# Kernel optimization log

Measured on AMD Instinct MI355X. Metric: run time of the kernel, lower is better.

## Reference

```python
import jax, jax.numpy as jnp
from jax import lax
import numpy as np

LRELU_SLOPE = 0.01  # PyTorch LeakyReLU default
BETA = 0.25


def lrelu(x):
    return jnp.where(x >= 0, x, LRELU_SLOPE * x)


def conv2d(x, w, b, stride, pad):
    # x: [B,C,H,W], w: [Cout,Cin,k,k] (torch OIHW)
    y = lax.conv_general_dilated(x, w, (stride, stride), ((pad, pad), (pad, pad)),
                                 dimension_numbers=('NCHW', 'OIHW', 'NCHW'))
    return y + b[None, :, None, None]


def conv_transpose2d(x, w, b, stride, out_pad):
    # w: torch ConvTranspose2d weight [Cin,Cout,k,k]; implement as dilated conv
    # with spatially flipped kernel. out = (i-1)*stride + k + out_pad.
    wf = jnp.flip(w, (2, 3)).transpose(1, 0, 2, 3)  # -> [Cout,Cin,k,k]
    k = w.shape[2]
    pad = ((k - 1, k - 1 + out_pad), (k - 1, k - 1 + out_pad))
    y = lax.conv_general_dilated(x, wf, (1, 1), pad, lhs_dilation=(stride, stride),
                                 dimension_numbers=('NCHW', 'OIHW', 'NCHW'))
    return y + b[None, :, None, None]


def setup_inputs() -> dict:
    key = jax.random.key(0)
    ks = jax.random.split(key, 16)
    s = 0.05
    inp = {
        'x':   jax.random.normal(ks[0], (64, 1, 256, 256), jnp.float32),
        'ew1': jax.random.normal(ks[1], (8, 1, 4, 4), jnp.float32) * s,
        'eb1': jnp.zeros((8,), jnp.float32),
        'ew2': jax.random.normal(ks[2], (16, 8, 4, 4), jnp.float32) * s,
        'eb2': jnp.zeros((16,), jnp.float32),
        'ew3': jax.random.normal(ks[3], (32, 16, 4, 4), jnp.float32) * s,
        'eb3': jnp.zeros((32,), jnp.float32),
        'ew4': jax.random.normal(ks[4], (32, 32, 3, 3), jnp.float32) * s,
        'eb4': jnp.zeros((32,), jnp.float32),
        'ew5': jax.random.normal(ks[5], (64, 32, 1, 1), jnp.float32) * s,
        'eb5': jnp.zeros((64,), jnp.float32),
        'dw1': jax.random.normal(ks[6], (32, 64, 3, 3), jnp.float32) * s,
        'db1': jnp.zeros((32,), jnp.float32),
        'dw2': jax.random.normal(ks[7], (32, 16, 4, 4), jnp.float32) * s,
        'db2': jnp.zeros((16,), jnp.float32),
        'dw3': jax.random.normal(ks[8], (16, 8, 4, 4), jnp.float32) * s,
        'db3': jnp.zeros((8,), jnp.float32),
        'dw4': jax.random.normal(ks[9], (8, 1, 4, 4), jnp.float32) * s,
        'db4': jnp.zeros((1,), jnp.float32),
        # nn.init.uniform_(-1/K, 1/K) with K=512
        'codebook': jax.random.uniform(ks[10], (512, 64), jnp.float32,
                                       minval=-1.0 / 512, maxval=1.0 / 512),
    }
    return inp


def vqvae_forward(x, ew1, eb1, ew2, eb2, ew3, eb3, ew4, eb4, ew5, eb5,
                  dw1, db1, dw2, db2, dw3, db3, dw4, db4, codebook):
    # ---- encoder ----
    h = lrelu(conv2d(x, ew1, eb1, 2, 0))   # [B,8,127,127]
    h = lrelu(conv2d(h, ew2, eb2, 2, 0))   # [B,16,62,62]
    h = lrelu(conv2d(h, ew3, eb3, 2, 0))   # [B,32,30,30]
    h = lrelu(conv2d(h, ew4, eb4, 1, 1))   # [B,32,30,30]
    h = lrelu(conv2d(h, ew5, eb5, 1, 0))   # [B,64,30,30]
    # ---- vector quantizer ----
    lat = h.transpose(0, 2, 3, 1)                      # [B,h,w,D]
    D = lat.shape[-1]
    flat = lat.reshape(-1, D)                          # [N,D]
    # squared euclidean distances via expansion (same argmin as torch.norm)
    d2 = (jnp.sum(flat * flat, axis=1, keepdims=True)
          - 2.0 * flat @ codebook.T
          + jnp.sum(codebook * codebook, axis=1))      # [N,K]
    idx = jnp.argmin(d2, axis=1)                       # [N]
    q = codebook[idx].reshape(lat.shape)               # [B,h,w,D]
    commitment = jnp.mean((lax.stop_gradient(q) - lat) ** 2)
    embedding = jnp.mean((q - lax.stop_gradient(lat)) ** 2)
    vq_loss = commitment * BETA + embedding
    q_st = lat + lax.stop_gradient(q - lat)            # straight-through
    z = q_st.transpose(0, 3, 1, 2)                     # [B,D,h,w]
    # ---- decoder ----
    h = lrelu(conv2d(z, dw1, db1, 1, 1))               # [B,32,30,30]
    h = lrelu(conv_transpose2d(h, dw2, db2, 2, 1))     # [B,16,63,63]
    h = lrelu(conv_transpose2d(h, dw3, db3, 2, 1))     # [B,8,131,131]
    recons = jnp.tanh(conv_transpose2d(h, dw4, db4, 2, 0))  # [B,1,264,264]
    return recons, vq_loss


def reference(x, ew1, eb1, ew2, eb2, ew3, eb3, ew4, eb4, ew5, eb5,
              dw1, db1, dw2, db2, dw3, db3, dw4, db4, codebook):
    return vqvae_forward(x, ew1, eb1, ew2, eb2, ew3, eb3, ew4, eb4, ew5, eb5,
                         dw1, db1, dw2, db2, dw3, db3, dw4, db4, codebook)
```

## Files before the change

### kernel.cpp

```cpp
#include <hip/hip_runtime.h>
#include <hip/hip_bf16.h>
#include <math.h>

#define LRELU 0.01f

template<int NW>
__device__ __forceinline__ void ldw(const float* p, float* w) {
    if constexpr (NW % 4 == 0) {
#pragma unroll
        for (int u = 0; u < NW / 4; u++) {
            float4 v = *(const float4*)(p + 4 * u);
            w[4*u] = v.x; w[4*u+1] = v.y; w[4*u+2] = v.z; w[4*u+3] = v.w;
        }
    } else {
#pragma unroll
        for (int c = 0; c < NW; c++) w[c] = p[c];
    }
}

__device__ __forceinline__ void wfwd(const float* s, float* d, int CIN, int COUT,
                                     int KK, int i) {
    int co = i / (CIN * KK); int r = i - co * CIN * KK;
    int ci = r / KK; int t = r - ci * KK;
    d[(ci * KK + t) * COUT + co] = s[i];
}
__device__ __forceinline__ void wtr(const float* s, float* d, int CIN, int COUT,
                                    int KK, int i) {
    int ci = i / (COUT * KK); int r = i - ci * COUT * KK;
    int co = r / KK; int t = r - co * KK;
    d[(t * CIN + ci) * COUT + co] = s[i];
}
__global__ __launch_bounds__(256)
void prep_k(const float* e1, const float* e2, const float* e3, const float* e4,
            const float* e5, const float* d1, const float* d2, const float* d3,
            const float* d4, float* w, const float* cbp, float* hcbn,
            unsigned long long* keys, float* loss, int* idxm, int N) {
    int i = blockIdx.x * 256 + threadIdx.x;
    if      (i < 128)   wfwd(e1, w + 0,     1,  8, 16, i);
    else if (i < 2176)  wfwd(e2, w + 128,   8, 16, 16, i - 128);
    else if (i < 10368) wfwd(e3, w + 2176, 16, 32, 16, i - 2176);
    else if (i < 19584) wfwd(e4, w + 10368, 32, 32, 9, i - 10368);
    else if (i < 21632) wfwd(e5, w + 19584, 32, 64, 1, i - 19584);
    else if (i < 40064) wfwd(d1, w + 21632, 64, 32, 9, i - 21632);
    else if (i < 48256) wtr (d2, w + 40064, 32, 16, 16, i - 40064);
    else if (i < 50304) wtr (d3, w + 48256, 16,  8, 16, i - 48256);
    else if (i < 50432) wtr (d4, w + 50304,  8,  1, 16, i - 50304);
    else if (i < 50944) {
        int k = i - 50432;
        const float* c = cbp + k * 64;
        float s = 0.f;
#pragma unroll
        for (int d = 0; d < 64; d++) s = fmaf(c[d], c[d], s);
        hcbn[k] = 0.5f * s;
    } else if (i < 50944 + N) {
        keys[i - 50944] = 0xFFFFFFFFFFFFFFFFull;
    } else if (i == 50944 + N) {
        loss[0] = 0.f;
    } else if (i < 50945 + N + 64 * 124) {
        int j = i - (50945 + N);
        int b2 = j / 124, s = j - b2 * 124;
        int r, c;
        if (s < 32)      { r = 0;  c = s; }
        else if (s < 64) { r = 31; c = s - 32; }
        else { int u = s - 64; r = 1 + (u >> 1); c = (u & 1) * 31; }
        idxm[b2 * 1024 + r * 32 + c] = 512;
    }
}

__global__ __launch_bounds__(256)
void ubuild_k(const float* __restrict__ w, const float* __restrict__ cb,
              float* __restrict__ U) {
    int g = blockIdx.x * 256 + threadIdx.x;
    if (g >= 513 * 288) return;
    if (g >= 512 * 288) { U[g] = 0.f; return; }
    int k = g / 288, rem = g - k * 288;
    const float* cr = cb + k * 64;
    float s = 0.f;
#pragma unroll 4
    for (int ci = 0; ci < 64; ci++)
        s = fmaf(w[ci * 288 + rem], cr[ci], s);
    U[g] = s;
}

template<int CIN, int COUT, int CO_BLK, int HIN, int ISTR, int HOUT, int WOUT,
         int OPLANE, int OSTR, int OPAD, int CB, int RB, int ZCONV, int ZF_CH>
__global__ __launch_bounds__(256)
void convs2_k(const float* __restrict__ in, const float* __restrict__ wt,
              const float* __restrict__ bias, float* __restrict__ out) {
    const int b = blockIdx.x, cog = blockIdx.y, tid = threadIdx.x;
    if (ZF_CH > 0 && (int)blockIdx.z >= ZCONV) {
        if (cog != 0) return;
        int i = ((int)blockIdx.z - ZCONV) * 256 + tid;
        if (i >= ZF_CH * 124) return;
        int ch = i / 124, s = i - ch * 124;
        int r, c;
        if (s < 32)      { r = 0;  c = s; }
        else if (s < 64) { r = 31; c = s - 32; }
        else { int u = s - 64; r = 1 + (u >> 1); c = (u & 1) * 31; }
        out[(size_t)(b * ZF_CH + ch) * 1024 + r * 32 + c] = 0.f;
        return;
    }
    __shared__ __align__(16) float lw[CIN * 16 * CO_BLK];
    for (int i = tid; i < CIN * 16 * CO_BLK; i += 256) {
        int row = i / CO_BLK, c = i - row * CO_BLK;
        lw[i] = wt[row * COUT + cog * CO_BLK + c];
    }
    __syncthreads();

    const int tz = blockIdx.z;
    const int cbi = tz / RB, rb = tz - cbi * RB;
    const int tx = tid & 15, ty = tid >> 4;
    const int ow0 = (cbi * 16 + tx) * 2;
    const int oh  = rb * 16 + ty;
    if (oh >= HOUT || ow0 >= WOUT) return;
    const bool p1v = (ow0 + 1) < WOUT;

    float acc[CO_BLK][2];
#pragma unroll
    for (int c = 0; c < CO_BLK; c++) {
        float bv = bias[cog * CO_BLK + c];
        acc[c][0] = bv; acc[c][1] = bv;
    }
    const float* inb = in + ((size_t)(b * CIN) * HIN + oh * 2) * ISTR + ow0 * 2;
#pragma unroll 2
    for (int ci = 0; ci < CIN; ci++) {
        const float* r = inb + (size_t)ci * HIN * ISTR;
        float4 a4[4]; float2 b2[4];
#pragma unroll
        for (int kh = 0; kh < 4; kh++) {
            a4[kh] = *(const float4*)(r + kh * ISTR);
            b2[kh] = p1v ? *(const float2*)(r + kh * ISTR + 4) : make_float2(0.f, 0.f);
        }
        const float* wr = lw + ci * 16 * CO_BLK;
#pragma unroll
        for (int kh = 0; kh < 4; kh++) {
            float x0[4] = {a4[kh].x, a4[kh].y, a4[kh].z, a4[kh].w};
            float x1[4] = {a4[kh].z, a4[kh].w, b2[kh].x, b2[kh].y};
#pragma unroll
            for (int kw = 0; kw < 4; kw++) {
                float wv[CO_BLK];
                ldw<CO_BLK>(wr + (kh * 4 + kw) * CO_BLK, wv);
#pragma unroll
                for (int c = 0; c < CO_BLK; c++) {
                    acc[c][0] = fmaf(x0[kw], wv[c], acc[c][0]);
                    acc[c][1] = fmaf(x1[kw], wv[c], acc[c][1]);
                }
            }
        }
    }
    float* ob = out + (size_t)(b * COUT + cog * CO_BLK) * OPLANE
                    + (oh + OPAD) * OSTR + ow0 + OPAD;
#pragma unroll
    for (int c = 0; c < CO_BLK; c++) {
        float v0 = acc[c][0]; v0 = (v0 >= 0.f) ? v0 : LRELU * v0;
        ob[(size_t)c * OPLANE] = v0;
        if (p1v) {
            float v1 = acc[c][1]; v1 = (v1 >= 0.f) ? v1 : LRELU * v1;
            ob[(size_t)c * OPLANE + 1] = v1;
        }
    }
}

template<int CIN, int COUT, int CO_BLK, int OPLANE, int OSTR, int OPADH, int OPADV,
         bool ZSIDE>
__global__ __launch_bounds__(256)
void conv3_k(const float* __restrict__ in, const float* __restrict__ wt,
             const float* __restrict__ bias, float* __restrict__ out) {
    const int b = blockIdx.x, cog = blockIdx.y, tid = threadIdx.x;
    __shared__ __align__(16) float lw[CIN * 9 * CO_BLK];
    for (int i = tid; i < CIN * 9 * CO_BLK; i += 256) {
        int row = i / CO_BLK, c = i - row * CO_BLK;
        lw[i] = wt[row * COUT + cog * CO_BLK + c];
    }
    __syncthreads();

    const int rb = blockIdx.z;
    const int tx = tid & 15, ty = tid >> 4;
    const int r = rb * 16 + ty;
    if (r >= 30) return;
    const int ow0 = tx * 2;
    if (tx == 15) {
        if (ZSIDE) {
#pragma unroll
            for (int c = 0; c < CO_BLK; c++) {
                float* base = out + (size_t)(b * COUT + cog * CO_BLK + c) * OPLANE
                                  + (r + OPADV) * OSTR;
                base[0] = 0.f; base[31] = 0.f; base[32] = 0.f;
            }
        }
        return;
    }
    float acc[CO_BLK][2];
#pragma unroll
    for (int c = 0; c < CO_BLK; c++) {
        float bv = bias[cog * CO_BLK + c];
        acc[c][0] = bv; acc[c][1] = bv;
    }
    const float* inb = in + ((size_t)(b * CIN) * 32 + r) * 32 + ow0;
#pragma unroll 2
    for (int ci = 0; ci < CIN; ci++) {
        const float* rr = inb + (size_t)ci * 1024;
        float2 A[3], Bv[3];
#pragma unroll
        for (int kh = 0; kh < 3; kh++) {
            A[kh]  = *(const float2*)(rr + kh * 32);
            Bv[kh] = *(const float2*)(rr + kh * 32 + 2);
        }
        const float* wr = lw + ci * 9 * CO_BLK;
#pragma unroll
        for (int kh = 0; kh < 3; kh++) {
            float x0[3] = {A[kh].x, A[kh].y, Bv[kh].x};
            float x1[3] = {A[kh].y, Bv[kh].x, Bv[kh].y};
#pragma unroll
            for (int kw = 0; kw < 3; kw++) {
                float wv[CO_BLK];
                ldw<CO_BLK>(wr + (kh * 3 + kw) * CO_BLK, wv);
#pragma unroll
                for (int c = 0; c < CO_BLK; c++) {
                    acc[c][0] = fmaf(x0[kw], wv[c], acc[c][0]);
                    acc[c][1] = fmaf(x1[kw], wv[c], acc[c][1]);
                }
            }
        }
    }
    float* ob = out + (size_t)(b * COUT + cog * CO_BLK) * OPLANE
                    + (r + OPADV) * OSTR + ow0 + OPADH;
#pragma unroll
    for (int c = 0; c < CO_BLK; c++) {
        float v0 = acc[c][0]; v0 = (v0 >= 0.f) ? v0 : LRELU * v0;
        float v1 = acc[c][1]; v1 = (v1 >= 0.f) ? v1 : LRELU * v1;
        ob[(size_t)c * OPLANE] = v0;
        ob[(size_t)c * OPLANE + 1] = v1;
    }
}

__global__ __launch_bounds__(256)
void conv1nhwc_k(const float* __restrict__ in, const float* __restrict__ wt,
                 const float* __restrict__ bias, float* __restrict__ latf) {
    __shared__ __align__(16) float lw[32 * 4];
    const int b = blockIdx.x, cog = blockIdx.y;
    for (int i = threadIdx.x; i < 32 * 4; i += 256) {
        int row = i / 4, c = i - row * 4;
        lw[i] = wt[row * 64 + cog * 4 + c];
    }
    __syncthreads();

    const int px4 = threadIdx.x * 4;
    float acc[4][4];
#pragma unroll
    for (int c = 0; c < 4; c++) {
        float bv = bias[cog * 4 + c];
        acc[c][0] = bv; acc[c][1] = bv; acc[c][2] = bv; acc[c][3] = bv;
    }
#pragma unroll 4
    for (int ci = 0; ci < 32; ci++) {
        float4 x = *(const float4*)(in + (size_t)(b * 32 + ci) * 1024 + px4);
        float wv[4];
        ldw<4>(lw + ci * 4, wv);
#pragma unroll
        for (int c = 0; c < 4; c++) {
            acc[c][0] = fmaf(x.x, wv[c], acc[c][0]);
            acc[c][1] = fmaf(x.y, wv[c], acc[c][1]);
            acc[c][2] = fmaf(x.z, wv[c], acc[c][2]);
            acc[c][3] = fmaf(x.w, wv[c], acc[c][3]);
        }
    }
#pragma unroll
    for (int j = 0; j < 4; j++) {
        int pix = px4 + j;
        int row = pix >> 5, col = pix & 31;
        if (row >= 1 && row <= 30 && col >= 1 && col <= 30) {
            int pos = b * 900 + (row - 1) * 30 + (col - 1);
            float4 v;
            v.x = (acc[0][j] >= 0.f) ? acc[0][j] : LRELU * acc[0][j];
            v.y = (acc[1][j] >= 0.f) ? acc[1][j] : LRELU * acc[1][j];
            v.z = (acc[2][j] >= 0.f) ? acc[2][j] : LRELU * acc[2][j];
            v.w = (acc[3][j] >= 0.f) ? acc[3][j] : LRELU * acc[3][j];
            *(float4*)(latf + (size_t)pos * 64 + cog * 4) = v;
        }
    }
}

__global__ __launch_bounds__(256)
void d1tab_k(const int* __restrict__ idxm, const float* __restrict__ U,
             const float* __restrict__ bias, float* __restrict__ out) {
    const int b = blockIdx.x, cog = blockIdx.y, rt = blockIdx.z;
    const int tx = threadIdx.x & 31, ty = threadIdx.x >> 5;
    const int r = rt * 8 + ty;
    if (r >= 30) return;
    if (tx >= 30) {
        if (tx == 31) {
#pragma unroll
            for (int c = 0; c < 16; c++) {
                float* base = out + (size_t)(b * 32 + cog * 16 + c) * 1020 + r * 34;
                base[1] = 0.f; base[32] = 0.f; base[33] = 0.f;
            }
        }
        return;
    }
    const int* im = idxm + b * 1024 + r * 32 + tx;
    float acc[16];
#pragma unroll
    for (int c = 0; c < 16; c++) acc[c] = bias[cog * 16 + c];
#pragma unroll
    for (int kh = 0; kh < 3; kh++) {
        int i0 = im[kh * 32 + 0];
        int i1 = im[kh * 32 + 1];
        int i2 = im[kh * 32 + 2];
        const float4* u0 = (const float4*)(U + ((size_t)i0 * 9 + kh * 3 + 0) * 32 + cog * 16);
        const float4* u1 = (const float4*)(U + ((size_t)i1 * 9 + kh * 3 + 1) * 32 + cog * 16);
        const float4* u2 = (const float4*)(U + ((size_t)i2 * 9 + kh * 3 + 2) * 32 + cog * 16);
#pragma unroll
        for (int q = 0; q < 4; q++) {
            float4 a = u0[q], bb = u1[q], cc = u2[q];
            acc[4*q+0] += (a.x + bb.x) + cc.x;
            acc[4*q+1] += (a.y + bb.y) + cc.y;
            acc[4*q+2] += (a.z + bb.z) + cc.z;
            acc[4*q+3] += (a.w + bb.w) + cc.w;
        }
    }
    float* ob = out + (size_t)(b * 32 + cog * 16) * 1020 + r * 34 + tx + 2;
#pragma unroll
    for (int c = 0; c < 16; c++) {
        float v = acc[c]; v = (v >= 0.f) ? v : LRELU * v;
        ob[(size_t)c * 1020] = v;
    }
}

template<int CIN, int COUT, int CO_BLK, int HIN, int ISTR, int HOUT, int WOUT,
         int OPLANE, int OSTR, int OPADH, int NTX, int NT,
         int ZS_CH, int ZS_H, int ZS_STR, int ZC0, int ZC1, int ZC2,
         bool DO_TANH, bool DO_LOSS>
__global__ __launch_bounds__(256)
void convtf_k(const float* __restrict__ in, const float* __restrict__ wt,
              const float* __restrict__ bias, float* __restrict__ out,
              const float* __restrict__ loss, float* __restrict__ losstgt) {
    const int b = blockIdx.x, tid = threadIdx.x;
    const int NCOG = COUT / CO_BLK;
    int zz = blockIdx.z;
    if (zz >= NCOG * NT) {
        if (DO_LOSS) {
            if (b == 0 && tid == 0)
                losstgt[0] = 1.25f * loss[0] / (57600.f * 64.f);
            return;
        }
        int i = (zz - NCOG * NT) * 256 + tid;
        if (i >= ZS_CH * ZS_H * 3) return;
        int ch = i / (ZS_H * 3); int u = i - ch * ZS_H * 3;
        int r = u / 3, c3 = u - r * 3;
        int col = (c3 == 0) ? ZC0 : (c3 == 1) ? ZC1 : ZC2;
        out[((size_t)(b * ZS_CH + ch) * ZS_H + r) * ZS_STR + col] = 0.f;
        return;
    }
    const int cog = zz / NT, tile = zz - cog * NT;
    const int tlx = tile % NTX, tly = tile / NTX;

    __shared__ __align__(16) float lw[16 * CIN * CO_BLK];
    for (int i = tid; i < 16 * CIN * CO_BLK; i += 256) {
        int aq = i / (CIN * 4 * CO_BLK);
        int r1 = i - aq * (CIN * 4 * CO_BLK);
        int ci = r1 / (4 * CO_BLK);
        int u  = r1 - ci * (4 * CO_BLK);
        int pp = u / CO_BLK, c = u - pp * CO_BLK;
        int a = aq >> 1, q = aq & 1, py = pp >> 1, px = pp & 1;
        int tap = (py + 2 * a) * 4 + px + 2 * q;
        lw[i] = wt[((size_t)tap * CIN + ci) * COUT + cog * CO_BLK + c];
    }
    __syncthreads();

    const int SX = (WOUT + 1) >> 1, SY = (HOUT + 1) >> 1;
    const int sx0 = tlx * 32 + (tid & 15);
    const int sx1 = sx0 + 16;
    const int sy  = tly * 16 + (tid >> 4);
    const bool v0 = sx0 < SX, v1 = sx1 < SX;
    if (sy >= SY || !(v0 || v1)) return;

    const bool rvA = (sy < HIN);
    const bool rvB = (sy >= 1) && (sy <= HIN);

    float acc[2][4][CO_BLK];
#pragma unroll
    for (int s = 0; s < 2; s++)
#pragma unroll
        for (int o = 0; o < 4; o++)
#pragma unroll
            for (int c = 0; c < CO_BLK; c++)
                acc[s][o][c] = bias[cog * CO_BLK + c];

    const float* base = in + (size_t)(b * CIN) * HIN * ISTR;
#pragma unroll 2
    for (int ci = 0; ci < CIN; ci++) {
        const float* rowA = base + (size_t)ci * HIN * ISTR + (size_t)sy * ISTR;
        const float* rowB = rowA - ISTR;
        float rA0x = 0.f, rA0y = 0.f, rA1x = 0.f, rA1y = 0.f;
        float rB0x = 0.f, rB0y = 0.f, rB1x = 0.f, rB1y = 0.f;
        if (rvA) {
            if (v0) { rA0x = rowA[sx0]; rA0y = rowA[sx0 + 1]; }
            if (v1) { rA1x = rowA[sx1]; rA1y = rowA[sx1 + 1]; }
        }
        if (rvB) {
            if (v0) { rB0x = rowB[sx0]; rB0y = rowB[sx0 + 1]; }
            if (v1) { rB1x = rowB[sx1]; rB1y = rowB[sx1 + 1]; }
        }
#pragma unroll
        for (int a = 0; a < 2; a++) {
#pragma unroll
            for (int q = 0; q < 2; q++) {
                float iv0 = q ? (a ? rB0x : rA0x) : (a ? rB0y : rA0y);
                float iv1 = q ? (a ? rB1x : rA1x) : (a ? rB1y : rA1y);
                const float* wp = lw + (size_t)((a * 2 + q) * CIN + ci) * (4 * CO_BLK);
                float wv[4 * CO_BLK];
                ldw<4 * CO_BLK>(wp, wv);
#pragma unroll
                for (int o = 0; o < 4; o++)
#pragma unroll
                    for (int c = 0; c < CO_BLK; c++) {
                        acc[0][o][c] = fmaf(iv0, wv[o * CO_BLK + c], acc[0][o][c]);
                        acc[1][o][c] = fmaf(iv1, wv[o * CO_BLK + c], acc[1][o][c]);
                    }
            }
        }
    }
#pragma unroll
    for (int s = 0; s < 2; s++) {
        if (s ? !v1 : !v0) continue;
        const int sxx = s ? sx1 : sx0;
        const int ow = 2 * sxx;
        const bool full = (ow + 1) < WOUT;
#pragma unroll
        for (int py = 0; py < 2; py++) {
            int oh = 2 * sy + py;
            if (oh >= HOUT) continue;
            float* ob = out + (size_t)(b * COUT + cog * CO_BLK) * OPLANE
                            + (size_t)oh * OSTR + ow + OPADH;
#pragma unroll
            for (int c = 0; c < CO_BLK; c++) {
                float va = acc[s][py * 2 + 0][c];
                float vb = acc[s][py * 2 + 1][c];
                if (DO_TANH) { va = tanhf(va); vb = tanhf(vb); }
                else {
                    va = (va >= 0.f) ? va : LRELU * va;
                    vb = (vb >= 0.f) ? vb : LRELU * vb;
                }
                if ((OPADH & 1) == 0 && full) {
                    *(float2*)(ob + (size_t)c * OPLANE) = make_float2(va, vb);
                } else {
                    ob[(size_t)c * OPLANE] = va;
                    if (full) ob[(size_t)c * OPLANE + 1] = vb;
                }
            }
        }
    }
}

__global__ __launch_bounds__(256, 4)
void vq_argmin_k(const float* __restrict__ latf, const float* __restrict__ cb,
                 const float* __restrict__ hcbn,
                 unsigned long long* __restrict__ keys) {
    const int pb = blockIdx.x;
    if (pb >= 225) return;
    const int pos = pb * 256 + threadIdx.x;
    const int kbase = blockIdx.y * 64;

    const float4* lp = (const float4*)(latf + (size_t)pos * 64);
    float4 L[16];
#pragma unroll
    for (int i = 0; i < 16; i++) L[i] = lp[i];

    float best = 3.4e38f;
    int   bi   = 0;
#pragma unroll 1
    for (int k = 0; k < 64; k++) {
        const float4* cp = (const float4*)(cb + (size_t)(kbase + k) * 64);
        float hn = hcbn[kbase + k];
        float a0 = 0.f, a1 = 0.f, a2 = 0.f, a3 = 0.f;
#pragma unroll
        for (int u = 0; u < 16; u++) {
            float4 c = cp[u];
            a0 = fmaf(L[u].x, c.x, a0);
            a1 = fmaf(L[u].y, c.y, a1);
            a2 = fmaf(L[u].z, c.z, a2);
            a3 = fmaf(L[u].w, c.w, a3);
        }
        float score = hn - ((a0 + a1) + (a2 + a3));
        if (score < best) { best = score; bi = kbase + k; }
    }
    unsigned u = __float_as_uint(best);
    u = ((int)u < 0) ? ~u : (u | 0x80000000u);
    unsigned long long key = ((unsigned long long)u << 32) | (unsigned)bi;
    atomicMin(&keys[pos], key);
}

__global__ __launch_bounds__(256)
void vq_finalize_k(const float* __restrict__ latf, const float* __restrict__ cb,
                   const unsigned long long* __restrict__ keys,
                   int* __restrict__ idxm, float* __restrict__ loss_acc, int B) {
    int gid = blockIdx.x * 256 + threadIdx.x;
    const int N = B * 900;
    float myloss = 0.f;
    if (gid < N) {
        int b = gid / 900, p = gid - b * 900;
        int oh = p / 30, ow = p - oh * 30;
        int pp = 33 + oh * 32 + ow;
        int idx = (int)(unsigned)(keys[gid] & 0xFFFFFFFFull);
        idxm[b * 1024 + pp] = idx;
        const float4* crow = (const float4*)(cb + (size_t)idx * 64);
        const float4* lrow = (const float4*)(latf + (size_t)gid * 64);
#pragma unroll
        for (int i = 0; i < 16; i++) {
            float4 cv = crow[i];
            float4 lv = lrow[i];
            float d0 = cv.x - lv.x, d1 = cv.y - lv.y;
            float d2 = cv.z - lv.z, d3 = cv.w - lv.w;
            myloss = fmaf(d0, d0, myloss);
            myloss = fmaf(d1, d1, myloss);
            myloss = fmaf(d2, d2, myloss);
            myloss = fmaf(d3, d3, myloss);
        }
    }
    __shared__ float red[256];
    red[threadIdx.x] = myloss;
    __syncthreads();
    for (int s = 128; s > 0; s >>= 1) {
        if ((int)threadIdx.x < s) red[threadIdx.x] += red[threadIdx.x + s];
        __syncthreads();
    }
    if (threadIdx.x == 0) atomicAdd(loss_acc, red[0]);
}

static inline int nblk(long long total) { return (int)((total + 255) / 256); }

extern "C" void kernel_launch(void* const* d_in, const int* in_sizes, int n_in,
                              void* d_out, int out_size, void* d_ws, size_t ws_size,
                              hipStream_t stream) {
    const float* x   = (const float*)d_in[0];
    const float* ew1 = (const float*)d_in[1];  const float* eb1 = (const float*)d_in[2];
    const float* ew2 = (const float*)d_in[3];  const float* eb2 = (const float*)d_in[4];
    const float* ew3 = (const float*)d_in[5];  const float* eb3 = (const float*)d_in[6];
    const float* ew4 = (const float*)d_in[7];  const float* eb4 = (const float*)d_in[8];
    const float* ew5 = (const float*)d_in[9];  const float* eb5 = (const float*)d_in[10];
    const float* dw1 = (const float*)d_in[11]; const float* db1 = (const float*)d_in[12];
    const float* dw2 = (const float*)d_in[13]; const float* db2 = (const float*)d_in[14];
    const float* dw3 = (const float*)d_in[15]; const float* db3 = (const float*)d_in[16];
    const float* dw4 = (const float*)d_in[17]; const float* db4 = (const float*)d_in[18];
    const float* cb  = (const float*)d_in[19];
    float* out = (float*)d_out;

    const int B = in_sizes[0] / (256 * 256);
    const int N = B * 900;

    char* ws = (char*)d_ws;
    float* A     = (float*)(ws);
    float* Bb    = (float*)(ws + 34873344);
    float* d2out = (float*)(ws + 34873344);
    float* d3out = (float*)(ws);
    unsigned long long* keys = (unsigned long long*)(ws + 51126272);
    float* hcbn  = (float*)(ws + 51587072);
    int*   idxm  = (int*)(ws + 51589120);
    float* loss  = (float*)(ws + 52420608);
    float* wtb   = (float*)(ws + 52420864);
    float* U     = (float*)(ws + 52622592);
    float* ew1t = wtb;          float* ew2t = wtb + 128;
    float* ew3t = wtb + 2176;   float* ew4t = wtb + 10368;
    float* ew5t = wtb + 19584;  float* dw1t = wtb + 21632;
    float* dw2t = wtb + 40064;  float* dw3t = wtb + 48256;
    float* dw4t = wtb + 50304;

    prep_k<<<nblk(50945 + N + 64 * 124), 256, 0, stream>>>(
        ew1, ew2, ew3, ew4, ew5, dw1, dw2, dw3, dw4, wtb,
        cb, hcbn, keys, loss, idxm, N);
    ubuild_k<<<nblk(513 * 288), 256, 0, stream>>>(dw1t, cb, U);

    convs2_k<1, 8, 8, 256, 256, 127, 127, 127 * 128, 128, 0, 4, 8, 32, 0>
        <<<dim3(B, 1, 32), 256, 0, stream>>>(x, ew1t, eb1, A);
    convs2_k<8, 16, 4, 127, 128, 62, 62, 62 * 64, 64, 0, 2, 4, 8, 0>
        <<<dim3(B, 4, 8), 256, 0, stream>>>(A, ew2t, eb2, Bb);
    convs2_k<16, 32, 4, 62, 64, 30, 30, 1024, 32, 1, 1, 2, 2, 32>
        <<<dim3(B, 8, 18), 256, 0, stream>>>(Bb, ew3t, eb3, A);
    conv3_k<32, 32, 4, 1024, 32, 1, 1, false>
        <<<dim3(B, 8, 2), 256, 0, stream>>>(A, ew4t, eb4, Bb);
    conv1nhwc_k<<<dim3(B, 16, 1), 256, 0, stream>>>(Bb, ew5t, eb5, A);

    vq_argmin_k<<<dim3(232, 8), 256, 0, stream>>>(A, cb, hcbn, keys);
    vq_finalize_k<<<nblk(N), 256, 0, stream>>>(A, cb, keys, idxm, loss, B);

    d1tab_k<<<dim3(B, 2, 4), 256, 0, stream>>>(idxm, U, db1, A);
    convtf_k<32, 16, 4, 30, 34, 63, 63, 63 * 68, 68, 2, 1, 2,
             16, 63, 68, 1, 65, 66, false, false>
        <<<dim3(B, 1, 20), 256, 0, stream>>>(A + 1, dw2t, db2, d2out,
                                             nullptr, nullptr);
    convtf_k<16, 8, 8, 63, 68, 129, 129, 129 * 132, 132, 2, 3, 15,
             8, 129, 132, 1, 1, 131, false, false>
        <<<dim3(B, 1, 28), 256, 0, stream>>>(d2out + 1, dw3t, db3, d3out,
                                             nullptr, nullptr);
    convtf_k<8, 1, 1, 129, 132, 260, 260, 67600, 260, 0, 5, 45,
             0, 1, 1, 0, 0, 0, true, true>
        <<<dim3(B, 1, 46), 256, 0, stream>>>(d3out + 1, dw4t, db4, out, loss,
                                             out + (out_size - 1));
}
```

Baseline: 414.1 us.

## Stage codebook slice in LDS and split VQ dot products across lane quads

The VQ argmin kernel now copies its 64-entry codebook slice and half-norms into shared memory once per block, instead of every thread reading them from global memory. Each group of four lanes shares the 64-dim dot product, with each lane covering 16 dims for four positions. Partial sums are combined with DPP quad-permute adds. This removes redundant global codebook traffic and cuts per-thread register use for the latent. The cost is extra shuffle instructions per candidate and possible LDS bank contention.

```diff
diff --git a/kernel.cpp b/kernel.cpp
--- a/kernel.cpp
+++ b/kernel.cpp
@@ -453,42 +453,79 @@
     }
 }
 
+template<int CTRL>
+__device__ __forceinline__ float dpp_qp_add(float x) {
+    int y = __builtin_amdgcn_update_dpp(0, __float_as_int(x), CTRL, 0xF, 0xF, true);
+    return x + __int_as_float(y);
+}
+
 __global__ __launch_bounds__(256, 4)
 void vq_argmin_k(const float* __restrict__ latf, const float* __restrict__ cb,
                  const float* __restrict__ hcbn,
                  unsigned long long* __restrict__ keys) {
     const int pb = blockIdx.x;
     if (pb >= 225) return;
-    const int pos = pb * 256 + threadIdx.x;
+    __shared__ float4 scb4[1024];
+    __shared__ float  shn[64];
+    const int tid = threadIdx.x;
+    const int dq  = tid & 3;
+    const int pg  = tid >> 2;
     const int kbase = blockIdx.y * 64;
-
-    const float4* lp = (const float4*)(latf + (size_t)pos * 64);
-    float4 L[16];
-#pragma unroll
-    for (int i = 0; i < 16; i++) L[i] = lp[i];
-
-    float best = 3.4e38f;
-    int   bi   = 0;
-#pragma unroll 1
+    const int posbase = pb * 256;
+
+    const float4* src = (const float4*)(cb + (size_t)kbase * 64);
+#pragma unroll
+    for (int i = 0; i < 4; i++) scb4[tid + 256 * i] = src[tid + 256 * i];
+    if (tid < 64) shn[tid] = hcbn[kbase + tid];
+
+    float4 L[4][4];
+    int pidx[4];
+#pragma unroll
+    for (int j = 0; j < 4; j++) {
+        int pos = posbase + pg + 64 * j;
+        pidx[j] = pos;
+        const float4* lp = (const float4*)(latf + (size_t)pos * 64 + dq * 16);
+#pragma unroll
+        for (int u = 0; u < 4; u++) L[j][u] = lp[u];
+    }
+    __syncthreads();
+
+    float best[4] = {3.4e38f, 3.4e38f, 3.4e38f, 3.4e38f};
+    int   bi[4]   = {0, 0, 0, 0};
+#pragma unroll 2
     for (int k = 0; k < 64; k++) {
-        const float4* cp = (const float4*)(cb + (size_t)(kbase + k) * 64);
-        float hn = hcbn[kbase + k];
-        float a0 = 0.f, a1 = 0.f, a2 = 0.f, a3 = 0.f;
-#pragma unroll
-        for (int u = 0; u < 16; u++) {
-            float4 c = cp[u];
-            a0 = fmaf(L[u].x, c.x, a0);
-            a1 = fmaf(L[u].y, c.y, a1);
-            a2 = fmaf(L[u].z, c.z, a2);
-            a3 = fmaf(L[u].w, c.w, a3);
-        }
-        float score = hn - ((a0 + a1) + (a2 + a3));
-        if (score < best) { best = score; bi = kbase + k; }
-    }
-    unsigned u = __float_as_uint(best);
-    u = ((int)u < 0) ? ~u : (u | 0x80000000u);
-    unsigned long long key = ((unsigned long long)u << 32) | (unsigned)bi;
-    atomicMin(&keys[pos], key);
+        float4 c0 = scb4[(k << 4) + (dq << 2) + 0];
+        float4 c1 = scb4[(k << 4) + (dq << 2) + 1];
+        float4 c2 = scb4[(k << 4) + (dq << 2) + 2];
+        float4 c3 = scb4[(k << 4) + (dq << 2) + 3];
+        float hn = shn[k];
+#pragma unroll
+        for (int j = 0; j < 4; j++) {
+            float a0 = 0.f, a1 = 0.f;
+            a0 = fmaf(L[j][0].x, c0.x, a0); a1 = fmaf(L[j][0].y, c0.y, a1);
+            a0 = fmaf(L[j][0].z, c0.z, a0); a1 = fmaf(L[j][0].w, c0.w, a1);
+            a0 = fmaf(L[j][1].x, c1.x, a0); a1 = fmaf(L[j][1].y, c1.y, a1);
+            a0 = fmaf(L[j][1].z, c1.z, a0); a1 = fmaf(L[j][1].w, c1.w, a1);
+            a0 = fmaf(L[j][2].x, c2.x, a0); a1 = fmaf(L[j][2].y, c2.y, a1);
+            a0 = fmaf(L[j][2].z, c2.z, a0); a1 = fmaf(L[j][2].w, c2.w, a1);
+            a0 = fmaf(L[j][3].x, c3.x, a0); a1 = fmaf(L[j][3].y, c3.y, a1);
+            a0 = fmaf(L[j][3].z, c3.z, a0); a1 = fmaf(L[j][3].w, c3.w, a1);
+            float dot = a0 + a1;
+            float t   = dpp_qp_add<0xB1>(dot);
+            float tot = dpp_qp_add<0x4E>(t);
+            float score = hn - tot;
+            if (score < best[j]) { best[j] = score; bi[j] = kbase + k; }
+        }
+    }
+    if (dq == 0) {
+#pragma unroll
+        for (int j = 0; j < 4; j++) {
+            unsigned u = __float_as_uint(best[j]);
+            u = ((int)u < 0) ? ~u : (u | 0x80000000u);
+            unsigned long long key = ((unsigned long long)u << 32) | (unsigned)bi[j];
+            atomicMin(&keys[pidx[j]], key);
+        }
+    }
 }
 
 __global__ __launch_bounds__(256)
```

Measured after the change: 410.0 us. Within noise of the previous version (-1.0%).
